# Performance work log

Hardware: AMD Instinct MI355X
Metric: run time of the kernel (lower is better)

## Reference

```python
import jax, jax.numpy as jnp
import numpy as np

# Module hyperparameters (from init_kwargs)
M = 2049          # NpointsMesh (odd)
TAU = 3e-6        # Gaussian spreading width
XLIMS = (0.0, 1.0)
MU0 = 1.0
L = abs(XLIMS[1] - XLIMS[0])
TWO_PI = 2.0 * np.pi
B, N = 16, 512


def _grids():
    kGrid = jnp.asarray(np.linspace(-(M // 2), M // 2, M), jnp.float32)
    xGrid = jnp.asarray(TWO_PI * np.linspace(XLIMS[0], XLIMS[1], M + 1)[:-1] / L, jnp.float32)
    return kGrid, xGrid


def setup_inputs() -> dict:
    key = jax.random.key(0)
    kx, = jax.random.split(key, 1)
    x = jax.random.uniform(kx, (B, N), dtype=jnp.float32)  # points inside xLims
    kGrid, _ = _grids()
    multRe0 = (4.0 * np.pi / (kGrid ** 2 + MU0 ** 2))[None, :].astype(jnp.float32)
    multRe1 = (4.0 * np.pi / (kGrid ** 2 + 1.0))[None, :].astype(jnp.float32)
    zeros = jnp.zeros((1, M), jnp.float32)
    return {"x": x, "multRe0": multRe0, "multIm0": zeros,
            "multRe1": multRe1, "multIm1": zeros}


def reference(x, multRe0, multIm0, multRe1, multIm1):
    kGrid, xGrid = _grids()
    # Gaussian spreading: (B, N, M)
    diff = x[..., None] * (TWO_PI / L) - xGrid
    g = jnp.exp(-(diff * diff) / (4.0 * TAU))
    red = jnp.sum(g, axis=1)  # (B, M)
    # NOTE: tf.signal.fftshift/ifftshift default to ALL axes; jnp matches that default.
    fftG = jnp.fft.fftshift(jnp.fft.fft(jax.lax.complex(red, jnp.zeros_like(red)))) * (L / TWO_PI)
    deconv = jnp.sqrt(np.pi / TAU) * jnp.exp((kGrid ** 2) * TAU)  # (M,) real
    rfft = fftG * deconv
    Re, Im = jnp.real(rfft), jnp.imag(rfft)

    def mix(mRe, mIm):
        # Faithful to source (incl. its naming quirk): real = mRe*Re - mRe*Im,
        # imag = mIm*Re + mIm*Im
        return jax.lax.complex(mRe * Re - mRe * Im, mIm * Re + mIm * Im)

    multFFT = jnp.stack([mix(multRe0, multIm0), mix(multRe1, multIm1)], axis=1)  # (B, 2, M)
    multDeconv = multFFT * deconv  # broadcast over (B, 2, M)
    irfft = jnp.real(jnp.fft.ifft(jnp.fft.ifftshift(multDeconv)))  # (B, 2, M)
    # local = irfft[:,None,:,:] * g[:,:,None,:]; fmm = sum over mesh / M  -> einsum
    fmm = jnp.einsum('bnm,bcm->bnc', g, irfft) / M  # (B, N, 2)
    return fmm
```

## Files before the change

kernel.cpp:

```cpp
#include <hip/hip_runtime.h>
#include <math.h>

#define MM 2049
#define BB 16
#define NN 512
#define JH 1025
#define JP 1040
#define SZ 8
#define PCH 128
#define JCH 5
#define Z2 4
#define JB2 257
#define TCH 5

static constexpr double D_TWO_PI    = 6.283185307179586476925286766559;
static constexpr double D_STEP      = D_TWO_PI / 2049.0;
static constexpr float  F_TWO_PI    = 6.28318530717958647692f;
static constexpr float  INV_4TAU    = 83333.33333333333f;
static constexpr float  PI_OVER_TAU = 1047197.5511965977f;
static constexpr float  TWO_TAU     = 6.0e-6f;
static constexpr float  INV_2PI     = 0.15915494309189533f;
static constexpr float  INV_M       = 1.0f / 2049.0f;
static constexpr float  WINF        = 8.0f;

__global__ void k_sdft1(const float* __restrict__ x, float2* __restrict__ PSp) {
    __shared__ float  LA[PCH];
    __shared__ float  LB[PCH];
    __shared__ float2 SD[PCH];
    __shared__ float  Lz;
    const int b  = blockIdx.y;
    const int z  = blockIdx.z;
    const int a0 = 1 + PCH * z;
    const int b0 = 2049 - PCH * (z + 1);
    for (int i = threadIdx.x; i < PCH; i += 256) { LA[i] = 0.0f; LB[i] = 0.0f; }
    if (threadIdx.x == 0) Lz = 0.0f;
    __syncthreads();
    for (int n = threadIdx.x; n < NN; n += 256) {
        float xv = x[b * NN + n];
        float xa = xv * F_TWO_PI;
        float p  = xv * (float)MM;
        int m0 = (int)ceilf(p - WINF);  if (m0 < 0) m0 = 0;
        int m1 = (int)floorf(p + WINF); if (m1 > MM - 1) m1 = MM - 1;
        bool hitA = (m1 >= a0) && (m0 <= a0 + PCH - 1);
        bool hitB = (m1 >= b0) && (m0 <= b0 + PCH - 1);
        bool hit0 = (z == 0) && (m0 == 0);
        if (!(hitA || hitB || hit0)) continue;
        for (int m = m0; m <= m1; ++m) {
            float xg = (float)((double)m * D_STEP);
            float d  = xa - xg;
            float g  = expf(-(d * d) * INV_4TAU);
            unsigned ia = (unsigned)(m - a0);
            unsigned ib = (unsigned)(m - b0);
            if (ia < PCH) atomicAdd(&LA[ia], g);
            if (ib < PCH) atomicAdd(&LB[ib], g);
            if (hit0 && m == 0) atomicAdd(&Lz, g);
        }
    }
    __syncthreads();
    for (int i = threadIdx.x; i < PCH; i += 256) {
        float ra = LA[i], rb = LB[PCH - 1 - i];
        SD[i] = make_float2(ra + rb, ra - rb);
    }
    __syncthreads();
    const int j = blockIdx.x * 256 + threadIdx.x;
    if (j >= JH) return;
    float ct, st;
    { float ang = (float)((double)j * D_STEP); __sincosf(ang, &st, &ct); }
    float c, s;
    { int r0 = (j * a0) % MM; float ph = (float)((double)r0 * D_STEP); __sincosf(ph, &s, &c); }
    float accc = 0.0f, accs = 0.0f;
    #pragma unroll 4
    for (int i = 0; i < PCH; ++i) {
        float2 sd = SD[i];
        accc = fmaf(sd.x, c, accc);
        accs = fmaf(sd.y, s, accs);
        float t1 = s * st, t2 = s * ct;
        float cn = fmaf(c, ct, -t1);
        float sn = fmaf(c, st,  t2);
        c = cn; s = sn;
    }
    if (z == 0) accc += Lz;
    PSp[((size_t)b * SZ + z) * JP + j] = make_float2(accc, accs);
}

__global__ void k_dft2m(const float2* __restrict__ PSp,
                        const float* __restrict__ mRe0, const float* __restrict__ mIm0,
                        const float* __restrict__ mRe1, const float* __restrict__ mIm1,
                        float* __restrict__ irfp) {
    __shared__ float4 lab[JB2];
    const int b   = blockIdx.y;
    const int zj  = blockIdx.z;
    const int jb0 = zj * JB2;
    const int jb1 = min(jb0 + JB2, JH);
    const int cntj = jb1 - jb0;
    for (int i = threadIdx.x; i < cntj; i += 256) {
        const int j = jb0 + i;
        float cs = 0.0f, sn = 0.0f;
        const float2* base = PSp + (size_t)b * SZ * JP + j;
        #pragma unroll
        for (int z = 0; z < SZ; ++z) {
            float2 ps = base[(size_t)z * JP];
            cs += ps.x; sn += ps.y;
        }
        const int msh = j + 1024;
        const float jf = (float)j;
        const float d2 = PI_OVER_TAU * expf(jf * jf * TWO_TAU);
        const float fac = (j == 0) ? 1.0f : 2.0f;
        const float sc = INV_2PI * d2 * fac;
        float4 v;
        v.x =  sc * mRe1[msh] * cs;
        v.y =  sc * mRe0[msh] * cs;
        v.z = -sc * mIm1[msh] * sn;
        v.w = -sc * mIm0[msh] * sn;
        lab[i] = v;
    }
    __syncthreads();
    const int t = blockIdx.x * 256 + threadIdx.x;
    if (t >= JH) return;
    float ct, st;
    { float ang = (float)((double)t * D_STEP); __sincosf(ang, &st, &ct); }
    float c, s;
    { int r0 = (t * jb0) % MM; float ph = (float)((double)r0 * D_STEP); __sincosf(ph, &s, &c); }
    float E0 = 0.0f, O0 = 0.0f, E1 = 0.0f, O1 = 0.0f;
    #pragma unroll 4
    for (int i = 0; i < cntj; ++i) {
        float4 v = lab[i];
        E0 = fmaf(v.x, c, E0);
        O0 = fmaf(v.z, s, O0);
        E1 = fmaf(v.y, c, E1);
        O1 = fmaf(v.w, s, O1);
        float t1 = s * st, t2 = s * ct;
        float cn = fmaf(c, ct, -t1);
        float sn2 = fmaf(c, st,  t2);
        c = cn; s = sn2;
    }
    float* o = irfp + ((size_t)(zj * BB + b) * MM) * 2;
    o[t * 2 + 0] = (E0 - O0) * INV_M;
    o[t * 2 + 1] = (E1 - O1) * INV_M;
    if (t >= 1) {
        o[(MM - t) * 2 + 0] = (E0 + O0) * INV_M;
        o[(MM - t) * 2 + 1] = (E1 + O1) * INV_M;
    }
}

__global__ void k_gather(const float* __restrict__ x, const float* __restrict__ irfp,
                         float* __restrict__ out) {
    const int idx = blockIdx.x * blockDim.x + threadIdx.x;
    if (idx >= BB * NN) return;
    const int b = idx / NN;
    float xv = x[idx];
    float xa = xv * F_TWO_PI;
    float p  = xv * (float)MM;
    int m0 = (int)ceilf(p - WINF);  if (m0 < 0) m0 = 0;
    int m1 = (int)floorf(p + WINF); if (m1 > MM - 1) m1 = MM - 1;
    float acc0 = 0.0f, acc1 = 0.0f;
    for (int m = m0; m <= m1; ++m) {
        float xg = (float)((double)m * D_STEP);
        float d  = xa - xg;
        float g  = expf(-(d * d) * INV_4TAU);
        float p0 = 0.0f, p1 = 0.0f;
        #pragma unroll
        for (int z = 0; z < Z2; ++z) {
            const float2* base = (const float2*)(irfp + ((size_t)(z * BB + b) * MM) * 2);
            float2 v = base[m];
            p0 += v.x;
            p1 += v.y;
        }
        acc0 = fmaf(g, p0, acc0);
        acc1 = fmaf(g, p1, acc1);
    }
    out[idx * 2 + 0] = acc0 * INV_M;
    out[idx * 2 + 1] = acc1 * INV_M;
}

extern "C" void kernel_launch(void* const* d_in, const int* in_sizes, int n_in,
                              void* d_out, int out_size, void* d_ws, size_t ws_size,
                              hipStream_t stream) {
    const float* x    = (const float*)d_in[0];
    const float* mRe0 = (const float*)d_in[1];
    const float* mIm0 = (const float*)d_in[2];
    const float* mRe1 = (const float*)d_in[3];
    const float* mIm1 = (const float*)d_in[4];
    float* out = (float*)d_out;

    float2* PSp  = (float2*)d_ws;
    float*  irfp = (float*)d_ws + (size_t)2 * BB * SZ * JP;

    k_sdft1 <<<dim3(JCH, BB, SZ), 256, 0, stream>>>(x, PSp);
    k_dft2m <<<dim3(TCH, BB, Z2), 256, 0, stream>>>(PSp, mRe0, mIm0, mRe1, mIm1, irfp);
    k_gather<<<(BB * NN + 255) / 256, 256, 0, stream>>>(x, irfp, out);
}
```

Before: 90.31 us.

## Fuse three stages into one cooperative kernel with grid syncs

Replaces the three kernel launches with a single cooperative kernel of 640 blocks that runs spreading plus the first DFT, the multiply plus inverse DFT, and the gather, separated by grid.sync. The second stage is split into 8 j-chunks instead of 4 so all blocks have work. The gather now uses 16 threads per point, combined with a shuffle reduction, instead of one thread per point. This removes launch gaps and gives the final stage more parallelism, at the cost of grid-wide barriers and a cooperative launch that falls back to the old three kernels if it fails.

```diff
diff --git a/kernel.cpp b/kernel.cpp
--- a/kernel.cpp
+++ b/kernel.cpp
@@ -1,5 +1,8 @@
 #include <hip/hip_runtime.h>
+#include <hip/hip_cooperative_groups.h>
 #include <math.h>
+
+namespace cg = cooperative_groups;
 
 #define MM 2049
 #define BB 16
@@ -9,9 +12,12 @@
 #define SZ 8
 #define PCH 128
 #define JCH 5
+#define TCH 5
 #define Z2 4
 #define JB2 257
-#define TCH 5
+#define Z2F 8
+#define JBF 129
+#define GRIDF 640
 
 static constexpr double D_TWO_PI    = 6.283185307179586476925286766559;
 static constexpr double D_STEP      = D_TWO_PI / 2049.0;
@@ -22,6 +28,182 @@
 static constexpr float  INV_2PI     = 0.15915494309189533f;
 static constexpr float  INV_M       = 1.0f / 2049.0f;
 static constexpr float  WINF        = 8.0f;
+
+
+struct P1S { float LA[PCH]; float LB[PCH]; float2 SD[PCH]; float Lz; };
+struct P2S { float4 lab[JBF]; };
+union ShU { P1S p1; P2S p2; };
+
+__global__ __launch_bounds__(256, 3)
+void k_fused(const float* __restrict__ x,
+             const float* __restrict__ mRe0, const float* __restrict__ mIm0,
+             const float* __restrict__ mRe1, const float* __restrict__ mIm1,
+             float2* __restrict__ PSp, float* __restrict__ irfp,
+             float* __restrict__ out) {
+    cg::grid_group grid = cg::this_grid();
+    __shared__ ShU sh;
+    const int flat = blockIdx.x;
+    const int tid  = threadIdx.x;
+
+    {
+        const int jc = flat % JCH;
+        const int b  = (flat / JCH) % BB;
+        const int z  = flat / (JCH * BB);
+        const int a0 = 1 + PCH * z;
+        const int b0 = 2049 - PCH * (z + 1);
+        for (int i = tid; i < PCH; i += 256) { sh.p1.LA[i] = 0.0f; sh.p1.LB[i] = 0.0f; }
+        if (tid == 0) sh.p1.Lz = 0.0f;
+        __syncthreads();
+        for (int n = tid; n < NN; n += 256) {
+            float xv = x[b * NN + n];
+            float xa = xv * F_TWO_PI;
+            float p  = xv * (float)MM;
+            int m0 = (int)ceilf(p - WINF);  if (m0 < 0) m0 = 0;
+            int m1 = (int)floorf(p + WINF); if (m1 > MM - 1) m1 = MM - 1;
+            bool hitA = (m1 >= a0) && (m0 <= a0 + PCH - 1);
+            bool hitB = (m1 >= b0) && (m0 <= b0 + PCH - 1);
+            bool hit0 = (z == 0) && (m0 == 0);
+            if (!(hitA || hitB || hit0)) continue;
+            for (int m = m0; m <= m1; ++m) {
+                float xg = (float)((double)m * D_STEP);
+                float d  = xa - xg;
+                float gw = expf(-(d * d) * INV_4TAU);
+                unsigned ia = (unsigned)(m - a0);
+                unsigned ib = (unsigned)(m - b0);
+                if (ia < PCH) atomicAdd(&sh.p1.LA[ia], gw);
+                if (ib < PCH) atomicAdd(&sh.p1.LB[ib], gw);
+                if (hit0 && m == 0) atomicAdd(&sh.p1.Lz, gw);
+            }
+        }
+        __syncthreads();
+        for (int i = tid; i < PCH; i += 256) {
+            float ra = sh.p1.LA[i], rb = sh.p1.LB[PCH - 1 - i];
+            sh.p1.SD[i] = make_float2(ra + rb, ra - rb);
+        }
+        __syncthreads();
+        const int j = jc * 256 + tid;
+        if (j < JH) {
+            float ct, st;
+            { float ang = (float)((double)j * D_STEP); __sincosf(ang, &st, &ct); }
+            float c, s;
+            { int r0 = (j * a0) % MM; float ph = (float)((double)r0 * D_STEP); __sincosf(ph, &s, &c); }
+            float accc = 0.0f, accs = 0.0f;
+            #pragma unroll 4
+            for (int i = 0; i < PCH; ++i) {
+                float2 sd = sh.p1.SD[i];
+                accc = fmaf(sd.x, c, accc);
+                accs = fmaf(sd.y, s, accs);
+                float t1 = s * st, t2 = s * ct;
+                float cn = fmaf(c, ct, -t1);
+                float sn = fmaf(c, st,  t2);
+                c = cn; s = sn;
+            }
+            if (z == 0) accc += sh.p1.Lz;
+            PSp[((size_t)b * SZ + z) * JP + j] = make_float2(accc, accs);
+        }
+    }
+    __threadfence();
+    grid.sync();
+
+    {
+        const int tc  = flat % TCH;
+        const int b   = (flat / TCH) % BB;
+        const int zj  = flat / (TCH * BB);
+        const int jb0 = zj * JBF;
+        const int jb1 = min(jb0 + JBF, JH);
+        const int cntj = jb1 - jb0;
+        for (int i = tid; i < cntj; i += 256) {
+            const int j = jb0 + i;
+            float cs = 0.0f, sn = 0.0f;
+            const float2* base = PSp + (size_t)b * SZ * JP + j;
+            #pragma unroll
+            for (int z = 0; z < SZ; ++z) {
+                float2 ps = base[(size_t)z * JP];
+                cs += ps.x; sn += ps.y;
+            }
+            const int msh = j + 1024;
+            const float jf = (float)j;
+            const float d2 = PI_OVER_TAU * expf(jf * jf * TWO_TAU);
+            const float fac = (j == 0) ? 1.0f : 2.0f;
+            const float sc = INV_2PI * d2 * fac;
+            float4 v;
+            v.x =  sc * mRe1[msh] * cs;
+            v.y =  sc * mRe0[msh] * cs;
+            v.z = -sc * mIm1[msh] * sn;
+            v.w = -sc * mIm0[msh] * sn;
+            sh.p2.lab[i] = v;
+        }
+        __syncthreads();
+        const int t = tc * 256 + tid;
+        if (t < JH) {
+            float ct, st;
+            { float ang = (float)((double)t * D_STEP); __sincosf(ang, &st, &ct); }
+            float c, s;
+            { int r0 = (t * jb0) % MM; float ph = (float)((double)r0 * D_STEP); __sincosf(ph, &s, &c); }
+            float E0 = 0.0f, O0 = 0.0f, E1 = 0.0f, O1 = 0.0f;
+            #pragma unroll 4
+            for (int i = 0; i < cntj; ++i) {
+                float4 v = sh.p2.lab[i];
+                E0 = fmaf(v.x, c, E0);
+                O0 = fmaf(v.z, s, O0);
+                E1 = fmaf(v.y, c, E1);
+                O1 = fmaf(v.w, s, O1);
+                float t1 = s * st, t2 = s * ct;
+                float cn = fmaf(c, ct, -t1);
+                float sn2 = fmaf(c, st,  t2);
+                c = cn; s = sn2;
+            }
+            float* o = irfp + ((size_t)(zj * BB + b) * MM) * 2;
+            o[t * 2 + 0] = (E0 - O0) * INV_M;
+            o[t * 2 + 1] = (E1 - O1) * INV_M;
+            if (t >= 1) {
+                o[(MM - t) * 2 + 0] = (E0 + O0) * INV_M;
+                o[(MM - t) * 2 + 1] = (E1 + O1) * INV_M;
+            }
+        }
+    }
+    __threadfence();
+    grid.sync();
+
+    {
+        const unsigned gg = (unsigned)flat * 256u + (unsigned)tid;
+        const unsigned p  = gg >> 4;
+        const unsigned tt = gg & 15u;
+        if (p < BB * NN) {
+            const int b = (int)p / NN;
+            float xv = x[p];
+            float xa = xv * F_TWO_PI;
+            float pp = xv * (float)MM;
+            int m0 = (int)ceilf(pp - WINF);  if (m0 < 0) m0 = 0;
+            int m1 = (int)floorf(pp + WINF); if (m1 > MM - 1) m1 = MM - 1;
+            float acc0 = 0.0f, acc1 = 0.0f;
+            for (int m = m0 + (int)tt; m <= m1; m += 16) {
+                float xg = (float)((double)m * D_STEP);
+                float d  = xa - xg;
+                float gw = expf(-(d * d) * INV_4TAU);
+                float p0 = 0.0f, p1 = 0.0f;
+                #pragma unroll
+                for (int z = 0; z < Z2F; ++z) {
+                    const float2* base = (const float2*)(irfp + ((size_t)(z * BB + b) * MM) * 2);
+                    float2 v = base[m];
+                    p0 += v.x;
+                    p1 += v.y;
+                }
+                acc0 = fmaf(gw, p0, acc0);
+                acc1 = fmaf(gw, p1, acc1);
+            }
+            #pragma unroll
+            for (int off = 8; off > 0; off >>= 1) {
+                acc0 += __shfl_xor(acc0, off);
+                acc1 += __shfl_xor(acc1, off);
+            }
+            if (tt == 0) {
+                out[p * 2 + 0] = acc0 * INV_M;
+                out[p * 2 + 1] = acc1 * INV_M;
+            }
+        }
+    }
+}
 
 __global__ void k_sdft1(const float* __restrict__ x, float2* __restrict__ PSp) {
     __shared__ float  LA[PCH];
@@ -186,7 +368,13 @@
     float2* PSp  = (float2*)d_ws;
     float*  irfp = (float*)d_ws + (size_t)2 * BB * SZ * JP;
 
-    k_sdft1 <<<dim3(JCH, BB, SZ), 256, 0, stream>>>(x, PSp);
-    k_dft2m <<<dim3(TCH, BB, Z2), 256, 0, stream>>>(PSp, mRe0, mIm0, mRe1, mIm1, irfp);
-    k_gather<<<(BB * NN + 255) / 256, 256, 0, stream>>>(x, irfp, out);
-}
+    void* args[] = { (void*)&x, (void*)&mRe0, (void*)&mIm0, (void*)&mRe1, (void*)&mIm1,
+                     (void*)&PSp, (void*)&irfp, (void*)&out };
+    hipError_t e = hipLaunchCooperativeKernel((const void*)k_fused, dim3(GRIDF), dim3(256),
+                                              (void**)args, 0u, stream);
+    if (e != hipSuccess) {
+        k_sdft1 <<<dim3(JCH, BB, SZ), 256, 0, stream>>>(x, PSp);
+        k_dft2m <<<dim3(TCH, BB, Z2), 256, 0, stream>>>(PSp, mRe0, mIm0, mRe1, mIm1, irfp);
+        k_gather<<<(BB * NN + 255) / 256, 256, 0, stream>>>(x, irfp, out);
+    }
+}
```

New measurement: 309.9 us. 243% more time.

## Fuse inverse DFT with gather kernel using shared-memory irfft slices and atomics

Applied to the files above, without the earlier changes.

Merges the inverse-DFT kernel and the gather kernel into one. Each block now computes a contiguous chunk of output mesh points (and their mirrored high half) over all frequencies, keeps them in shared memory, and gathers the Gaussian-weighted contributions for the points that touch that chunk. Results are accumulated into the output with atomics, and the output is zeroed inside the first kernel. This removes one launch and the global irfft round trip. In exchange each block does a full-length frequency loop with fewer active threads (205 of 256), there are only 80 blocks, and x is re-read by every block.

```diff
diff --git a/kernel.cpp b/kernel.cpp
--- a/kernel.cpp
+++ b/kernel.cpp
@@ -9,9 +9,8 @@
 #define SZ 8
 #define PCH 128
 #define JCH 5
-#define Z2 4
-#define JB2 257
-#define TCH 5
+#define CT2 205
+#define TCH2 5
 
 static constexpr double D_TWO_PI    = 6.283185307179586476925286766559;
 static constexpr double D_STEP      = D_TWO_PI / 2049.0;
@@ -23,7 +22,9 @@
 static constexpr float  INV_M       = 1.0f / 2049.0f;
 static constexpr float  WINF        = 8.0f;
 
-__global__ void k_sdft1(const float* __restrict__ x, float2* __restrict__ PSp) {
+
+__global__ void k_sdft1(const float* __restrict__ x, float2* __restrict__ PSp,
+                        float* __restrict__ out) {
     __shared__ float  LA[PCH];
     __shared__ float  LB[PCH];
     __shared__ float2 SD[PCH];
@@ -32,6 +33,9 @@
     const int z  = blockIdx.z;
     const int a0 = 1 + PCH * z;
     const int b0 = 2049 - PCH * (z + 1);
+    if (blockIdx.x == 0 && z == 0) {
+        for (int i = threadIdx.x; i < NN * 2; i += 256) out[b * NN * 2 + i] = 0.0f;
+    }
     for (int i = threadIdx.x; i < PCH; i += 256) { LA[i] = 0.0f; LB[i] = 0.0f; }
     if (threadIdx.x == 0) Lz = 0.0f;
     __syncthreads();
@@ -83,18 +87,21 @@
     PSp[((size_t)b * SZ + z) * JP + j] = make_float2(accc, accs);
 }
 
-__global__ void k_dft2m(const float2* __restrict__ PSp,
-                        const float* __restrict__ mRe0, const float* __restrict__ mIm0,
-                        const float* __restrict__ mRe1, const float* __restrict__ mIm1,
-                        float* __restrict__ irfp) {
-    __shared__ float4 lab[JB2];
+__global__ __launch_bounds__(256)
+void k_dft2g(const float2* __restrict__ PSp,
+             const float* __restrict__ mRe0, const float* __restrict__ mIm0,
+             const float* __restrict__ mRe1, const float* __restrict__ mIm1,
+             const float* __restrict__ x, float* __restrict__ out) {
+    __shared__ float4 lab[JH];
+    __shared__ float2 irfL[CT2];
+    __shared__ float2 irfH[CT2];
+    const int tc  = blockIdx.x;
     const int b   = blockIdx.y;
-    const int zj  = blockIdx.z;
-    const int jb0 = zj * JB2;
-    const int jb1 = min(jb0 + JB2, JH);
-    const int cntj = jb1 - jb0;
-    for (int i = threadIdx.x; i < cntj; i += 256) {
-        const int j = jb0 + i;
+    const int t0  = tc * CT2;
+    const int tid = threadIdx.x;
+
+    for (int i = tid; i < JH; i += 256) {
+        const int j = i;
         float cs = 0.0f, sn = 0.0f;
         const float2* base = PSp + (size_t)b * SZ * JP + j;
         #pragma unroll
@@ -115,62 +122,67 @@
         lab[i] = v;
     }
     __syncthreads();
-    const int t = blockIdx.x * 256 + threadIdx.x;
-    if (t >= JH) return;
-    float ct, st;
-    { float ang = (float)((double)t * D_STEP); __sincosf(ang, &st, &ct); }
-    float c, s;
-    { int r0 = (t * jb0) % MM; float ph = (float)((double)r0 * D_STEP); __sincosf(ph, &s, &c); }
-    float E0 = 0.0f, O0 = 0.0f, E1 = 0.0f, O1 = 0.0f;
-    #pragma unroll 4
-    for (int i = 0; i < cntj; ++i) {
-        float4 v = lab[i];
-        E0 = fmaf(v.x, c, E0);
-        O0 = fmaf(v.z, s, O0);
-        E1 = fmaf(v.y, c, E1);
-        O1 = fmaf(v.w, s, O1);
-        float t1 = s * st, t2 = s * ct;
-        float cn = fmaf(c, ct, -t1);
-        float sn2 = fmaf(c, st,  t2);
-        c = cn; s = sn2;
-    }
-    float* o = irfp + ((size_t)(zj * BB + b) * MM) * 2;
-    o[t * 2 + 0] = (E0 - O0) * INV_M;
-    o[t * 2 + 1] = (E1 - O1) * INV_M;
-    if (t >= 1) {
-        o[(MM - t) * 2 + 0] = (E0 + O0) * INV_M;
-        o[(MM - t) * 2 + 1] = (E1 + O1) * INV_M;
-    }
-}
-
-__global__ void k_gather(const float* __restrict__ x, const float* __restrict__ irfp,
-                         float* __restrict__ out) {
-    const int idx = blockIdx.x * blockDim.x + threadIdx.x;
-    if (idx >= BB * NN) return;
-    const int b = idx / NN;
-    float xv = x[idx];
-    float xa = xv * F_TWO_PI;
-    float p  = xv * (float)MM;
-    int m0 = (int)ceilf(p - WINF);  if (m0 < 0) m0 = 0;
-    int m1 = (int)floorf(p + WINF); if (m1 > MM - 1) m1 = MM - 1;
-    float acc0 = 0.0f, acc1 = 0.0f;
-    for (int m = m0; m <= m1; ++m) {
-        float xg = (float)((double)m * D_STEP);
-        float d  = xa - xg;
-        float g  = expf(-(d * d) * INV_4TAU);
-        float p0 = 0.0f, p1 = 0.0f;
-        #pragma unroll
-        for (int z = 0; z < Z2; ++z) {
-            const float2* base = (const float2*)(irfp + ((size_t)(z * BB + b) * MM) * 2);
-            float2 v = base[m];
-            p0 += v.x;
-            p1 += v.y;
-        }
-        acc0 = fmaf(g, p0, acc0);
-        acc1 = fmaf(g, p1, acc1);
-    }
-    out[idx * 2 + 0] = acc0 * INV_M;
-    out[idx * 2 + 1] = acc1 * INV_M;
+
+    if (tid < CT2) {
+        const int t = t0 + tid;
+        float ct, st;
+        { float ang = (float)((double)t * D_STEP); __sincosf(ang, &st, &ct); }
+        float E0 = 0.0f, O0 = 0.0f, E1 = 0.0f, O1 = 0.0f;
+        for (int q0 = 0; q0 < JH; q0 += 128) {
+            const int qe = min(q0 + 128, JH);
+            float c, s;
+            { int r0 = (t * q0) % MM; float ph = (float)((double)r0 * D_STEP); __sincosf(ph, &s, &c); }
+            #pragma unroll 4
+            for (int i = q0; i < qe; ++i) {
+                float4 v = lab[i];
+                E0 = fmaf(v.x, c, E0);
+                O0 = fmaf(v.z, s, O0);
+                E1 = fmaf(v.y, c, E1);
+                O1 = fmaf(v.w, s, O1);
+                float t1 = s * st, t2 = s * ct;
+                float cn = fmaf(c, ct, -t1);
+                float sn2 = fmaf(c, st,  t2);
+                c = cn; s = sn2;
+            }
+        }
+        irfL[tid] = make_float2((E0 - O0) * INV_M, (E1 - O1) * INV_M);
+        irfH[tid] = make_float2((E0 + O0) * INV_M, (E1 + O1) * INV_M);
+    }
+    __syncthreads();
+
+    const int L0 = t0, L1 = t0 + CT2 - 1;
+    const int H0 = MM - L1, H1 = MM - max(t0, 1);
+    for (int n = tid; n < NN; n += 256) {
+        const int p = b * NN + n;
+        float xv = x[p];
+        float xa = xv * F_TWO_PI;
+        float pp = xv * (float)MM;
+        int m0 = (int)ceilf(pp - WINF);  if (m0 < 0) m0 = 0;
+        int m1 = (int)floorf(pp + WINF); if (m1 > MM - 1) m1 = MM - 1;
+        float a0 = 0.0f, a1 = 0.0f;
+        int lo = max(m0, L0), hi = min(m1, L1);
+        for (int m = lo; m <= hi; ++m) {
+            float xg = (float)((double)m * D_STEP);
+            float d  = xa - xg;
+            float g  = expf(-(d * d) * INV_4TAU);
+            float2 v = irfL[m - L0];
+            a0 = fmaf(g, v.x, a0);
+            a1 = fmaf(g, v.y, a1);
+        }
+        int lo2 = max(m0, H0), hi2 = min(m1, H1);
+        for (int m = lo2; m <= hi2; ++m) {
+            float xg = (float)((double)m * D_STEP);
+            float d  = xa - xg;
+            float g  = expf(-(d * d) * INV_4TAU);
+            float2 v = irfH[(MM - m) - t0];
+            a0 = fmaf(g, v.x, a0);
+            a1 = fmaf(g, v.y, a1);
+        }
+        if ((hi >= lo) || (hi2 >= lo2)) {
+            atomicAdd(&out[p * 2 + 0], a0 * INV_M);
+            atomicAdd(&out[p * 2 + 1], a1 * INV_M);
+        }
+    }
 }
 
 extern "C" void kernel_launch(void* const* d_in, const int* in_sizes, int n_in,
@@ -183,10 +195,8 @@
     const float* mIm1 = (const float*)d_in[4];
     float* out = (float*)d_out;
 
-    float2* PSp  = (float2*)d_ws;
-    float*  irfp = (float*)d_ws + (size_t)2 * BB * SZ * JP;
-
-    k_sdft1 <<<dim3(JCH, BB, SZ), 256, 0, stream>>>(x, PSp);
-    k_dft2m <<<dim3(TCH, BB, Z2), 256, 0, stream>>>(PSp, mRe0, mIm0, mRe1, mIm1, irfp);
-    k_gather<<<(BB * NN + 255) / 256, 256, 0, stream>>>(x, irfp, out);
+    float2* PSp = (float2*)d_ws;
+
+    k_sdft1<<<dim3(JCH, BB, SZ), 256, 0, stream>>>(x, PSp, out);
+    k_dft2g<<<dim3(TCH2, BB), 256, 0, stream>>>(PSp, mRe0, mIm0, mRe1, mIm1, x, out);
 }
```

Result: slower. 106.2 us (+17.6%).
